# Optimization experiments

Hardware: AMD Instinct MI355X
Metric: run time of the kernel (lower is better)

The kernel has to match this reference:

```python
import jax, jax.numpy as jnp
import numpy as np

H, DK, DV, DM = 8, 64, 64, 512
MAX_REL = 32
REL_VOCAB = 2 * MAX_REL + 1  # use_neg_dist=True
TREE_VOCAB = 64


def rel_pos_matrix(length):
    r = jnp.arange(length)
    dist = r[None, :] - r[:, None]                      # [L, L]
    dist = jnp.clip(dist, -MAX_REL, MAX_REL)
    return dist + MAX_REL                               # use_neg_dist -> shift


def setup_inputs() -> dict:
    key = jax.random.key(0)
    ks = jax.random.split(key, 16)
    B, L = 8, 1024
    s = 0.02
    return {
        "key": jax.random.normal(ks[0], (B, L, DM), jnp.float32),
        "value": jax.random.normal(ks[1], (B, L, DM), jnp.float32),
        "query": jax.random.normal(ks[2], (B, L, DM), jnp.float32),
        "mask": jnp.zeros((B, L, L), jnp.bool_),
        "rel_matrix": jax.random.randint(ks[3], (B, L, L), 0, TREE_VOCAB, jnp.int32),
        "rel_mask": jax.random.uniform(ks[4], (B, L, L), jnp.float32),
        "Wk": jax.random.normal(ks[5], (DM, H * DK), jnp.float32) * s,
        "bk": jnp.zeros((H * DK,), jnp.float32),
        "Wq": jax.random.normal(ks[6], (DM, H * DK), jnp.float32) * s,
        "bq": jnp.zeros((H * DK,), jnp.float32),
        "Wv": jax.random.normal(ks[7], (DM, H * DV), jnp.float32) * s,
        "bv": jnp.zeros((H * DV,), jnp.float32),
        "Wo": jax.random.normal(ks[8], (H * DV, DM), jnp.float32) * s,
        "bo": jnp.zeros((DM,), jnp.float32),
        "rel_emb_k": jax.random.normal(ks[9], (REL_VOCAB, DK), jnp.float32) * s,
        "rel_emb_v": jax.random.normal(ks[10], (REL_VOCAB, DV), jnp.float32) * s,
        "tree_emb": jax.random.normal(ks[11], (TREE_VOCAB, H), jnp.float32) * s,
    }


def reference(key, value, query, mask, rel_matrix, rel_mask,
              Wk, bk, Wq, bq, Wv, bv, Wo, bo, rel_emb_k, rel_emb_v, tree_emb):
    B, L, _ = key.shape

    def shape(x, d):  # (B, L, H*d) -> (B, H, L, d)
        return x.reshape(B, L, H, d).transpose(0, 2, 1, 3)

    k = shape(key @ Wk + bk, DK)       # [B,H,L,DK]
    v = shape(value @ Wv + bv, DV)     # [B,H,L,DV]
    q = shape(query @ Wq + bq, DK)     # [B,H,L,DK]

    rp = rel_pos_matrix(L)             # [L,L] int constant
    rel_k = rel_emb_k[rp]              # [L,L,DK]
    rel_v = rel_emb_v[rp]              # [L,L,DV]

    q = q / jnp.sqrt(jnp.asarray(DK, q.dtype))
    scores = jnp.einsum("bhqd,bhkd->bhqk", q, k)
    # relative_matmul(q, rel_k, transpose=True)
    scores = scores + jnp.einsum("bhqd,qkd->bhqk", q, rel_k)
    # tree-relative bias: embedding lookup [B,Q,K,H] -> [B,H,Q,K], masked
    tree_bias = tree_emb[rel_matrix].transpose(0, 3, 1, 2)
    scores = scores + tree_bias * rel_mask[:, None, :, :]

    scores = scores.astype(jnp.float32)
    scores = jnp.where(mask[:, None, :, :], -1e18, scores)
    attn = jax.nn.softmax(scores, axis=-1).astype(q.dtype)  # [B,H,Q,K]

    ctx = jnp.einsum("bhqk,bhkd->bhqd", attn, v)
    # relative_matmul(attn, rel_v, transpose=False)
    ctx = ctx + jnp.einsum("bhqk,qkd->bhqd", attn, rel_v)

    ctx = ctx.transpose(0, 2, 1, 3).reshape(B, L, H * DV)
    return ctx @ Wo + bo
```

## Files before the change

### kernel.cpp

```cpp
#include <hip/hip_runtime.h>
#include <stdint.h>

using f32x4  = __attribute__((ext_vector_type(4))) float;
using short8 = __attribute__((ext_vector_type(8))) short;
typedef unsigned short u16;
typedef unsigned int   u32;


static __device__ __forceinline__ u16 f2bf(float f) {
  union { float f; u32 u; } v; v.f = f;
  u32 r = v.u + 0x7fffu + ((v.u >> 16) & 1u);
  return (u16)(r >> 16);
}
static __device__ __forceinline__ float bf2f(u16 u) {
  union { u32 u; float f; } v; v.u = ((u32)u) << 16;
  return v.f;
}
static __device__ __forceinline__ float fexp2(float x) {
  float r;
  asm("v_exp_f32 %0, %1" : "=v"(r) : "v"(x));
  return r;
}
static __device__ __forceinline__ u32 cvtpk(float a, float b) {
  u32 r;
  asm("v_cvt_pk_bf16_f32 %0, %1, %2" : "=v"(r) : "v"(a), "v"(b));
  return r;
}

#define GLDS16(g, l) __builtin_amdgcn_global_load_lds( \
    (const __attribute__((address_space(1))) u32*)(g), \
    (__attribute__((address_space(3))) u32*)(l), 16, 0, 0)

__global__ __launch_bounds__(256) void k_pre(
    const float* __restrict__ W0, const float* __restrict__ W1,
    const float* __restrict__ W2, const float* __restrict__ W3,
    u16* __restrict__ T0, u16* __restrict__ T1, u16* __restrict__ T2, u16* __restrict__ T3,
    const float* __restrict__ rk, const float* __restrict__ rv,
    u16* __restrict__ relk80, u16* __restrict__ relvT,
    const int* __restrict__ rm, const float* __restrict__ rw,
    const unsigned char* __restrict__ mk, u32* __restrict__ outp) {
  __shared__ float t[32][33];
  int bid = blockIdx.x, tid = threadIdx.x;
  if (bid < 1024) {
    int mat = bid >> 8, rem = bid & 255;
    const float* W = (mat == 0) ? W0 : (mat == 1) ? W1 : (mat == 2) ? W2 : W3;
    u16* T = (mat == 0) ? T0 : (mat == 1) ? T1 : (mat == 2) ? T2 : T3;
    int tx = tid & 31, ty = tid >> 5;
    int x0 = (rem & 15) * 32, y0 = (rem >> 4) * 32;
    #pragma unroll
    for (int i = 0; i < 4; i++)
      t[ty + i*8][tx] = W[(y0 + ty + i*8) * 512 + (x0 + tx)];
    __syncthreads();
    #pragma unroll
    for (int i = 0; i < 4; i++)
      T[(x0 + ty + i*8) * 512 + (y0 + tx)] = f2bf(t[tx][ty + i*8]);
  } else if (bid < 1068) {
    int i = (bid - 1024) * 256 + tid;
    if (i < 80*64) {
      int row = i >> 6;
      relk80[i] = (row < 65) ? f2bf(rk[i]) : (u16)0;
    }
    int j = i - 80*64;
    if (j >= 0 && j < 64*96) {
      int dv = j / 96, bk = j % 96;
      relvT[j] = (bk < 65) ? f2bf(rv[bk*64 + dv]) : (u16)0;
    }
  } else {
    int i = (bid - 1068) * 256 + tid;
    int4   r4 = ((const int4*)rm)[i];
    float4 w4 = ((const float4*)rw)[i];
    uchar4 m4 = ((const uchar4*)mk)[i];
    uint4 o;
    o.x = (u32)(r4.x & 63) | (m4.x ? 128u : 0u) | ((u32)f2bf(w4.x) << 16);
    o.y = (u32)(r4.y & 63) | (m4.y ? 128u : 0u) | ((u32)f2bf(w4.y) << 16);
    o.z = (u32)(r4.z & 63) | (m4.z ? 128u : 0u) | ((u32)f2bf(w4.z) << 16);
    o.w = (u32)(r4.w & 63) | (m4.w ? 128u : 0u) | ((u32)f2bf(w4.w) << 16);
    ((uint4*)outp)[i] = o;
  }
}

struct FArg { const float* A; const u16* Wt; const float* bias; void* out; int mode; float scale; };
struct GArg { const u16* A; const u16* Wt; const float* bias; void* out; int mode; float scale; };

__global__ __launch_bounds__(256, 3) void k_gemmf(FArg g0, FArg g1, FArg g2) {
  FArg ar = (blockIdx.z == 0) ? g0 : (blockIdx.z == 1) ? g1 : g2;
  __shared__ char smem_[34816];
  u16* As = (u16*)smem_;
  u16* Bs = (u16*)(smem_ + 16384);
  u16* Cs = (u16*)smem_;
  int tid = threadIdx.x, lane = tid & 63, wv = tid >> 6;
  int quad = lane >> 4, l15 = lane & 15;
  int n0 = blockIdx.x * 128, m0 = blockIdx.y * 128;
  int wm = (wv >> 1) * 64, wn = (wv & 1) * 64;
  f32x4 acc[4][4];
  #pragma unroll
  for (int i = 0; i < 4; i++)
    #pragma unroll
    for (int j = 0; j < 4; j++)
      acc[i][j] = (f32x4){0.f, 0.f, 0.f, 0.f};

  const float* Asrc = ar.A + (size_t)(m0 + (tid >> 1)) * 512 + (tid & 1) * 16;
  const u16* Bbase = ar.Wt + (size_t)n0 * 512;
  int c0 = wv * 128;

  float4 fA[4];
#define LOADA(kt) do { _Pragma("unroll") \
    for (int i = 0; i < 4; i++) fA[i] = *(const float4*)(Asrc + (kt)*32 + i*4); } while (0)
#define WRITEA(nb) do { \
    u32 w0 = cvtpk(fA[0].x, fA[0].y), w1 = cvtpk(fA[0].z, fA[0].w); \
    u32 w2 = cvtpk(fA[1].x, fA[1].y), w3 = cvtpk(fA[1].z, fA[1].w); \
    u32 w4 = cvtpk(fA[2].x, fA[2].y), w5 = cvtpk(fA[2].z, fA[2].w); \
    u32 w6 = cvtpk(fA[3].x, fA[3].y), w7 = cvtpk(fA[3].z, fA[3].w); \
    ((uint4*)&As[(nb)*4096 + tid*16])[0] = make_uint4(w0, w1, w2, w3); \
    ((uint4*)&As[(nb)*4096 + tid*16])[1] = make_uint4(w4, w5, w6, w7); } while (0)
#define GLDSB(kt, nb) do { _Pragma("unroll") \
    for (int i = 0; i < 2; i++) { \
      int c = c0 + i*64 + lane; \
      GLDS16(Bbase + (c >> 2)*512 + (kt)*32 + (c & 3)*8, &Bs[(nb)*4096 + (c0 + i*64)*8]); \
    } } while (0)

  LOADA(0);
  WRITEA(0);
  GLDSB(0, 0);

  for (int ks = 0; ks < 16; ks++) {
    int cur = ks & 1;
    if (ks < 15) LOADA(ks + 1);
    __syncthreads();
    if (ks < 15) { WRITEA(cur ^ 1); GLDSB(ks + 1, cur ^ 1); }
    int bs = cur * 4096;
    short8 af[4], bf[4];
    #pragma unroll
    for (int i = 0; i < 4; i++) af[i] = *(const short8*)&As[bs + (wm + i*16 + l15)*32 + quad*8];
    #pragma unroll
    for (int j = 0; j < 4; j++) bf[j] = *(const short8*)&Bs[bs + (wn + j*16 + l15)*32 + quad*8];
    __builtin_amdgcn_s_setprio(1);
    #pragma unroll
    for (int i = 0; i < 4; i++)
      #pragma unroll
      for (int j = 0; j < 4; j++)
        acc[i][j] = __builtin_amdgcn_mfma_f32_16x16x32_bf16(af[i], bf[j], acc[i][j], 0, 0, 0);
    __builtin_amdgcn_s_setprio(0);
  }
#undef LOADA
#undef WRITEA
#undef GLDSB
  __syncthreads();

  {
    #pragma unroll
    for (int i = 0; i < 4; i++)
      #pragma unroll
      for (int j = 0; j < 4; j++) {
        int nloc = wn + j*16 + l15;
        float bv = ar.bias[n0 + nloc];
        #pragma unroll
        for (int r = 0; r < 4; r++) {
          int mloc = wm + i*16 + quad*4 + r;
          float val = (acc[i][j][r] + bv) * ar.scale;
          if (ar.mode == 1) Cs[mloc*136 + nloc] = f2bf(val);
          else              Cs[nloc*136 + mloc] = f2bf(val);
        }
      }
    __syncthreads();
    int bb = m0 >> 10, hh0 = n0 >> 6, mbase = m0 & 1023;
    u16* outp = (u16*)ar.out;
    if (ar.mode == 1) {
      #pragma unroll
      for (int p = 0; p < 8; p++) {
        int mloc = (tid >> 4) + p*16, seg = tid & 15;
        int head = hh0 + (seg >> 3);
        size_t base = ((size_t)(bb*8 + head)*1024 + mbase)*64;
        *(short8*)(outp + base + (size_t)mloc*64 + (seg & 7)*8) =
            *(const short8*)&Cs[mloc*136 + seg*8];
      }
    } else {
      #pragma unroll
      for (int p = 0; p < 8; p++) {
        int nloc = (tid >> 4) + p*16, seg = tid & 15;
        int head = hh0 + (nloc >> 6), d = nloc & 63;
        size_t base = (size_t)(bb*8 + head)*64*1024 + mbase;
        *(short8*)(outp + base + (size_t)d*1024 + seg*8) =
            *(const short8*)&Cs[nloc*136 + seg*8];
      }
    }
  }
}

__global__ __launch_bounds__(256, 4) void k_gemm(GArg g0, GArg g1, GArg g2) {
  GArg ar = (blockIdx.z == 0) ? g0 : (blockIdx.z == 1) ? g1 : g2;
  __shared__ char smem_[34816];
  u16* As = (u16*)smem_;
  u16* Bs = (u16*)(smem_ + 16384);
  u16* Cs = (u16*)smem_;
  int tid = threadIdx.x, lane = tid & 63, wv = tid >> 6;
  int quad = lane >> 4, l15 = lane & 15;
  int n0 = blockIdx.x * 128, m0 = blockIdx.y * 128;
  int wm = (wv >> 1) * 64, wn = (wv & 1) * 64;
  f32x4 acc[4][4];
  #pragma unroll
  for (int i = 0; i < 4; i++)
    #pragma unroll
    for (int j = 0; j < 4; j++)
      acc[i][j] = (f32x4){0.f, 0.f, 0.f, 0.f};

  const u16* Abase = ar.A  + (size_t)m0 * 512;
  const u16* Bbase = ar.Wt + (size_t)n0 * 512;
  int c0 = wv * 128;

#define STAGEG(kt, nb) do { \
    _Pragma("unroll") \
    for (int i = 0; i < 2; i++) { \
      int c = c0 + i*64 + lane; \
      GLDS16(Abase + (c >> 2)*512 + (kt)*32 + (c & 3)*8, &As[(nb)*4096 + (c0 + i*64)*8]); \
      GLDS16(Bbase + (c >> 2)*512 + (kt)*32 + (c & 3)*8, &Bs[(nb)*4096 + (c0 + i*64)*8]); \
    } } while (0)

  STAGEG(0, 0);

  for (int ks = 0; ks < 16; ks++) {
    int cur = ks & 1;
    __syncthreads();
    if (ks < 15) STAGEG(ks + 1, cur ^ 1);
    int bs = cur * 4096;
    short8 af[4], bf[4];
    #pragma unroll
    for (int i = 0; i < 4; i++) af[i] = *(const short8*)&As[bs + (wm + i*16 + l15)*32 + quad*8];
    #pragma unroll
    for (int j = 0; j < 4; j++) bf[j] = *(const short8*)&Bs[bs + (wn + j*16 + l15)*32 + quad*8];
    __builtin_amdgcn_s_setprio(1);
    #pragma unroll
    for (int i = 0; i < 4; i++)
      #pragma unroll
      for (int j = 0; j < 4; j++)
        acc[i][j] = __builtin_amdgcn_mfma_f32_16x16x32_bf16(af[i], bf[j], acc[i][j], 0, 0, 0);
    __builtin_amdgcn_s_setprio(0);
  }
#undef STAGEG
  __syncthreads();

  if (ar.mode == 0) {
    #pragma unroll
    for (int i = 0; i < 4; i++)
      #pragma unroll
      for (int j = 0; j < 4; j++) {
        int ncol = n0 + wn + j*16 + l15;
        float bv = ar.bias[ncol];
        #pragma unroll
        for (int r = 0; r < 4; r++) {
          int m = m0 + wm + i*16 + quad*4 + r;
          ((float*)ar.out)[m*512 + ncol] = (acc[i][j][r] + bv) * ar.scale;
        }
      }
  } else {
    #pragma unroll
    for (int i = 0; i < 4; i++)
      #pragma unroll
      for (int j = 0; j < 4; j++) {
        int nloc = wn + j*16 + l15;
        float bv = ar.bias[n0 + nloc];
        #pragma unroll
        for (int r = 0; r < 4; r++) {
          int mloc = wm + i*16 + quad*4 + r;
          float val = (acc[i][j][r] + bv) * ar.scale;
          if (ar.mode == 1) Cs[mloc*136 + nloc] = f2bf(val);
          else              Cs[nloc*136 + mloc] = f2bf(val);
        }
      }
    __syncthreads();
    int bb = m0 >> 10, hh0 = n0 >> 6, mbase = m0 & 1023;
    u16* outp = (u16*)ar.out;
    if (ar.mode == 1) {
      #pragma unroll
      for (int p = 0; p < 8; p++) {
        int mloc = (tid >> 4) + p*16, seg = tid & 15;
        int head = hh0 + (seg >> 3);
        size_t base = ((size_t)(bb*8 + head)*1024 + mbase)*64;
        *(short8*)(outp + base + (size_t)mloc*64 + (seg & 7)*8) =
            *(const short8*)&Cs[mloc*136 + seg*8];
      }
    } else {
      #pragma unroll
      for (int p = 0; p < 8; p++) {
        int nloc = (tid >> 4) + p*16, seg = tid & 15;
        int head = hh0 + (nloc >> 6), d = nloc & 63;
        size_t base = (size_t)(bb*8 + head)*64*1024 + mbase;
        *(short8*)(outp + base + (size_t)d*1024 + seg*8) =
            *(const short8*)&Cs[nloc*136 + seg*8];
      }
    }
  }
}

__global__ __launch_bounds__(512, 4) void k_attn(
    const u16* __restrict__ qws, const u16* __restrict__ kws, const u16* __restrict__ vtws,
    const u16* __restrict__ relk80, const u16* __restrict__ relvT,
    const float* __restrict__ tree_emb, const u32* __restrict__ packed,
    u16* __restrict__ ctx) {
  __shared__ u16 Kb[2][2048];
  __shared__ u16 Vb[2][2048];
  __shared__ u16 qdotL[8*16*68];
  __shared__ u16 PB[8][16*96];
  __shared__ u16 Pl[8][16*40];

  int tid = threadIdx.x, lane = tid & 63, wv = tid >> 6;
  int quad = lane >> 4, l15 = lane & 15;
  int qb = blockIdx.x, h = blockIdx.y, b = blockIdx.z;
  int q0 = qb * 128 + wv * 16;

  float treev = tree_emb[lane * 8 + h] * 1.44269504f;

  #pragma unroll
  for (int i = 0; i < 12; i++) ((u32*)&PB[wv][0])[lane + i*64] = 0u;

  const u16* qp = qws  + (size_t)(b*8 + h)*(1024*64);
  const u16* kp = kws  + (size_t)(b*8 + h)*(1024*64);
  const u16* vp = vtws + (size_t)(b*8 + h)*(64*1024);
  const u32* pkb = packed + ((size_t)b << 20);

  int rk = (wv & 3)*8 + (lane >> 3);
  int swk = (((lane & 7)*8) ^ ((rk & 7) << 3));
  int rv = (wv & 3)*16 + (lane >> 2);
  const u16* vsrc = vp + (size_t)rv*1024 + (((lane & 3)*8) ^ ((rv & 3) << 3));

#define STAGE(kt, nb) do { \
    if (wv < 4) GLDS16(kp + (size_t)((kt)*32 + rk)*64 + swk, &Kb[nb][wv*512]); \
    else        GLDS16(vsrc + (kt)*32, &Vb[nb][(wv & 3)*512]); \
  } while (0)

  STAGE(0, 0);

  short8 aQ[2];
  #pragma unroll
  for (int kf = 0; kf < 2; kf++)
    aQ[kf] = *(const short8*)(qp + (q0 + l15)*64 + kf*32 + quad*8);

  float qd0[4], qd64[4];
  #pragma unroll
  for (int t = 0; t < 5; t++) {
    f32x4 C = (f32x4){0.f,0.f,0.f,0.f};
    #pragma unroll
    for (int kf = 0; kf < 2; kf++) {
      short8 bR = *(const short8*)(relk80 + (t*16 + l15)*64 + kf*32 + quad*8);
      C = __builtin_amdgcn_mfma_f32_16x16x32_bf16(aQ[kf], bR, C, 0, 0, 0);
    }
    if (t == 0) {
      #pragma unroll
      for (int r = 0; r < 4; r++) qd0[r] = __shfl(C[r], lane & 48, 64);
    }
    if (t == 4) {
      #pragma unroll
      for (int r = 0; r < 4; r++) qd64[r] = __shfl(C[r], lane & 48, 64);
    }
    int col = t*16 + l15;
    if (col < 65) {
      #pragma unroll
      for (int r = 0; r < 4; r++)
        qdotL[(wv*16 + quad*4 + r)*68 + col] = f2bf(C[r]);
    }
  }

  int t_lo = max(0, (q0 - 31) >> 5);
  int t_hi = min(31, (q0 + 46) >> 5);

  int sK = (l15 & 7) << 3;
  int kbo0 = l15*64 + ((quad*8) ^ sK);
  int kbo1 = l15*64 + (((4 + quad)*8) ^ sK);
  int vbo  = l15*32 + ((quad*8) ^ ((l15 & 3) << 3));

  u32 pk[8];
  #pragma unroll
  for (int e = 0; e < 8; e++)
    pk[e] = pkb[((q0 + quad*4 + (e & 3)) << 10) + (e >> 2)*16 + l15];

  f32x4 O[4];
  float rs[4], ts0[4], ts1[4];
  #pragma unroll
  for (int t = 0; t < 4; t++) O[t] = (f32x4){0.f,0.f,0.f,0.f};
  #pragma unroll
  for (int r = 0; r < 4; r++) { rs[r] = 0.f; ts0[r] = 0.f; ts1[r] = 0.f; }

  for (int jt = 0; jt < 32; ++jt) {
    int cur = jt & 1;
    int k0 = jt << 5;
    __syncthreads();
    if (jt < 31) STAGE(jt + 1, cur ^ 1);

    u32 pkc[8];
    #pragma unroll
    for (int e = 0; e < 8; e++) pkc[e] = pk[e];
    if (jt < 31) {
      int kn = (jt + 1) << 5;
      #pragma unroll
      for (int e = 0; e < 8; e++)
        pk[e] = pkb[((q0 + quad*4 + (e & 3)) << 10) + kn + (e >> 2)*16 + l15];
    }

    short8 kr00 = *(const short8*)&Kb[cur][kbo0];
    short8 kr01 = *(const short8*)&Kb[cur][kbo1];
    short8 kr10 = *(const short8*)&Kb[cur][1024 + kbo0];
    short8 kr11 = *(const short8*)&Kb[cur][1024 + kbo1];
    short8 vr[4];
    #pragma unroll
    for (int t = 0; t < 4; t++) vr[t] = *(const short8*)&Vb[cur][t*512 + vbo];

    f32x4 S0 = (f32x4){0.f,0.f,0.f,0.f}, S1 = (f32x4){0.f,0.f,0.f,0.f};
    __builtin_amdgcn_s_setprio(1);
    S0 = __builtin_amdgcn_mfma_f32_16x16x32_bf16(aQ[0], kr00, S0, 0, 0, 0);
    S0 = __builtin_amdgcn_mfma_f32_16x16x32_bf16(aQ[1], kr01, S0, 0, 0, 0);
    S1 = __builtin_amdgcn_mfma_f32_16x16x32_bf16(aQ[0], kr10, S1, 0, 0, 0);
    S1 = __builtin_amdgcn_mfma_f32_16x16x32_bf16(aQ[1], kr11, S1, 0, 0, 0);
    __builtin_amdgcn_s_setprio(0);
    f32x4 Scur[2] = { S0, S1 };

    if (jt < t_lo) {
      #pragma unroll
      for (int ct = 0; ct < 2; ct++) {
        float pv[4];
        #pragma unroll
        for (int r = 0; r < 4; r++) {
          u32 sg = pkc[ct*4 + r];
          float rw = __uint_as_float(sg & 0xffff0000u);
          float tb = __int_as_float(__builtin_amdgcn_ds_bpermute(
              (int)((sg & 63u) << 2), __float_as_int(treev)));
          float qm = (sg & 128u) ? -1e30f : qd0[r];
          float p = fexp2(__builtin_fmaf(tb, rw, Scur[ct][r] + qm));
          ts0[r] += p;
          pv[r] = p;
        }
        u32 c01 = cvtpk(pv[0], pv[1]), c23 = cvtpk(pv[2], pv[3]);
        u16* pl = &Pl[wv][(quad*4)*40 + ct*16 + l15];
        pl[0]   = (u16)c01; pl[40]  = (u16)(c01 >> 16);
        pl[80]  = (u16)c23; pl[120] = (u16)(c23 >> 16);
      }
    } else if (jt > t_hi) {
      #pragma unroll
      for (int ct = 0; ct < 2; ct++) {
        float pv[4];
        #pragma unroll
        for (int r = 0; r < 4; r++) {
          u32 sg = pkc[ct*4 + r];
          float rw = __uint_as_float(sg & 0xffff0000u);
          float tb = __int_as_float(__builtin_amdgcn_ds_bpermute(
              (int)((sg & 63u) << 2), __float_as_int(treev)));
          float qm = (sg & 128u) ? -1e30f : qd64[r];
          float p = fexp2(__builtin_fmaf(tb, rw, Scur[ct][r] + qm));
          ts1[r] += p;
          pv[r] = p;
        }
        u32 c01 = cvtpk(pv[0], pv[1]), c23 = cvtpk(pv[2], pv[3]);
        u16* pl = &Pl[wv][(quad*4)*40 + ct*16 + l15];
        pl[0]   = (u16)c01; pl[40]  = (u16)(c01 >> 16);
        pl[80]  = (u16)c23; pl[120] = (u16)(c23 >> 16);
      }
    } else {
      #pragma unroll
      for (int ct = 0; ct < 2; ct++) {
        float pv[4];
        #pragma unroll
        for (int r = 0; r < 4; r++) {
          int kloc = ct*16 + l15, qloc = quad*4 + r;
          int d = (k0 + kloc) - (q0 + qloc);
          int bucket = min(max(d + 32, 0), 64);
          u32 sg = pkc[ct*4 + r];
          float rw = __uint_as_float(sg & 0xffff0000u);
          float tb = __int_as_float(__builtin_amdgcn_ds_bpermute(
              (int)((sg & 63u) << 2), __float_as_int(treev)));
          float qd = bf2f(qdotL[(wv*16 + qloc)*68 + bucket]);
          float qm = (sg & 128u) ? -1e30f : qd;
          float p = fexp2(__builtin_fmaf(tb, rw, Scur[ct][r] + qm));
          if (d <= -32)      ts0[r] += p;
          else if (d >= 32)  ts1[r] += p;
          else             { rs[r] += p; PB[wv][qloc*96 + d + 32] = f2bf(p); }
          pv[r] = p;
        }
        u32 c01 = cvtpk(pv[0], pv[1]), c23 = cvtpk(pv[2], pv[3]);
        u16* pl = &Pl[wv][(quad*4)*40 + ct*16 + l15];
        pl[0]   = (u16)c01; pl[40]  = (u16)(c01 >> 16);
        pl[80]  = (u16)c23; pl[120] = (u16)(c23 >> 16);
      }
    }

    {
      short8 aP = *(const short8*)&Pl[wv][l15*40 + quad*8];
      __builtin_amdgcn_s_setprio(1);
      #pragma unroll
      for (int t = 0; t < 4; t++)
        O[t] = __builtin_amdgcn_mfma_f32_16x16x32_bf16(aP, vr[t], O[t], 0, 0, 0);
      __builtin_amdgcn_s_setprio(0);
    }
  }
#undef STAGE

  #pragma unroll
  for (int m = 1; m < 16; m <<= 1) {
    #pragma unroll
    for (int r = 0; r < 4; r++) {
      rs[r]  += __shfl_xor(rs[r],  m, 64);
      ts0[r] += __shfl_xor(ts0[r], m, 64);
      ts1[r] += __shfl_xor(ts1[r], m, 64);
    }
  }
  if (l15 == 0) {
    #pragma unroll
    for (int r = 0; r < 4; r++) {
      PB[wv][(quad*4 + r)*96 + 0]  = f2bf(ts0[r]);
      PB[wv][(quad*4 + r)*96 + 64] = f2bf(ts1[r]);
    }
  }

  {
    short8 aB[3];
    #pragma unroll
    for (int s = 0; s < 3; s++)
      aB[s] = *(const short8*)&PB[wv][l15*96 + s*32 + quad*8];
    #pragma unroll
    for (int t = 0; t < 4; t++)
      #pragma unroll
      for (int s = 0; s < 3; s++) {
        short8 bRV = *(const short8*)(relvT + (t*16 + l15)*96 + s*32 + quad*8);
        O[t] = __builtin_amdgcn_mfma_f32_16x16x32_bf16(aB[s], bRV, O[t], 0, 0, 0);
      }
  }

  {
    float inv[4];
    #pragma unroll
    for (int r = 0; r < 4; r++) inv[r] = 1.0f / (rs[r] + ts0[r] + ts1[r]);
    #pragma unroll
    for (int t = 0; t < 4; t++)
      #pragma unroll
      for (int r = 0; r < 4; r++) {
        int qg = q0 + quad*4 + r;
        ctx[(b*1024 + qg)*512 + h*64 + t*16 + l15] = f2bf(O[t][r] * inv[r]);
      }
  }
}

extern "C" void kernel_launch(void* const* d_in, const int* in_sizes, int n_in,
                              void* d_out, int out_size, void* d_ws, size_t ws_size,
                              hipStream_t stream) {
  const float* key   = (const float*)d_in[0];
  const float* value = (const float*)d_in[1];
  const float* query = (const float*)d_in[2];
  const unsigned char* maskp = (const unsigned char*)d_in[3];
  const int*   relm  = (const int*)d_in[4];
  const float* relw  = (const float*)d_in[5];
  const float* Wk = (const float*)d_in[6];
  const float* bk = (const float*)d_in[7];
  const float* Wq = (const float*)d_in[8];
  const float* bq = (const float*)d_in[9];
  const float* Wv = (const float*)d_in[10];
  const float* bv = (const float*)d_in[11];
  const float* Wo = (const float*)d_in[12];
  const float* bo = (const float*)d_in[13];
  const float* rek = (const float*)d_in[14];
  const float* rev = (const float*)d_in[15];
  const float* te  = (const float*)d_in[16];
  (void)in_sizes; (void)n_in; (void)out_size;

  char* w = (char*)d_ws;
  size_t off = 0;
  auto alloc = [&](size_t bytes) -> void* {
    void* p = w + off; off += (bytes + 255) & ~(size_t)255; return p;
  };
  u16* WkT = (u16*)alloc((size_t)512*512*2);
  u16* WqT = (u16*)alloc((size_t)512*512*2);
  u16* WvT = (u16*)alloc((size_t)512*512*2);
  u16* WoT = (u16*)alloc((size_t)512*512*2);
  u16* qws = (u16*)alloc((size_t)8*8*1024*64*2);
  u16* kws = (u16*)alloc((size_t)8*8*1024*64*2);
  u16* vt  = (u16*)alloc((size_t)8*8*1024*64*2);
  u32* packed = (u32*)alloc((size_t)8*1024*1024*4);
  u16* ctxb = (u16*)alloc((size_t)8192*512*2);
  u16* relk80 = (u16*)alloc((size_t)80*64*2);
  u16* relvT  = (u16*)alloc((size_t)64*96*2);
  if (off > ws_size) return;

  k_pre<<<9260, 256, 0, stream>>>(Wk, Wq, Wv, Wo, WkT, WqT, WvT, WoT,
                                  rek, rev, relk80, relvT,
                                  relm, relw, maskp, packed);

  FArg aq { query, WqT, bq, (void*)qws, 1, 0.18033688f };
  FArg ak { key,   WkT, bk, (void*)kws, 1, 1.0f };
  FArg av { value, WvT, bv, (void*)vt,  2, 1.0f };
  k_gemmf<<<dim3(4,64,3), 256, 0, stream>>>(aq, ak, av);

  k_attn<<<dim3(8,8,8), 512, 0, stream>>>(qws, kws, vt, relk80, relvT, te, packed, ctxb);

  GArg ao { ctxb, WoT, bo, d_out, 0, 1.0f };
  k_gemm<<<dim3(4,64,1), 256, 0, stream>>>(ao, ao, ao);
}
```

Baseline: 287.1 us.

## Move mask packing into QKV GEMM launch and deepen A-tile prefetch

The packing of rel_matrix, rel_mask and mask into one 32-bit word per element moves out of the preprocessing kernel and into extra blocks of the QKV projection GEMM launch. The bandwidth-bound packing can then run alongside the compute-bound GEMM blocks instead of before them. The GEMM main loop also gains a second fp32 A register buffer and is unrolled by two, so global loads for A are issued two k-steps ahead. This adds register pressure and places heavy and light blocks in a single grid.

```diff
diff --git a/kernel.cpp b/kernel.cpp
--- a/kernel.cpp
+++ b/kernel.cpp
@@ -36,9 +36,7 @@
     const float* __restrict__ W2, const float* __restrict__ W3,
     u16* __restrict__ T0, u16* __restrict__ T1, u16* __restrict__ T2, u16* __restrict__ T3,
     const float* __restrict__ rk, const float* __restrict__ rv,
-    u16* __restrict__ relk80, u16* __restrict__ relvT,
-    const int* __restrict__ rm, const float* __restrict__ rw,
-    const unsigned char* __restrict__ mk, u32* __restrict__ outp) {
+    u16* __restrict__ relk80, u16* __restrict__ relvT) {
   __shared__ float t[32][33];
   int bid = blockIdx.x, tid = threadIdx.x;
   if (bid < 1024) {
@@ -54,7 +52,7 @@
     #pragma unroll
     for (int i = 0; i < 4; i++)
       T[(x0 + ty + i*8) * 512 + (y0 + tx)] = f2bf(t[tx][ty + i*8]);
-  } else if (bid < 1068) {
+  } else {
     int i = (bid - 1024) * 256 + tid;
     if (i < 80*64) {
       int row = i >> 6;
@@ -65,8 +63,18 @@
       int dv = j / 96, bk = j % 96;
       relvT[j] = (bk < 65) ? f2bf(rv[bk*64 + dv]) : (u16)0;
     }
-  } else {
-    int i = (bid - 1068) * 256 + tid;
+  }
+}
+
+struct FArg { const float* A; const u16* Wt; const float* bias; void* out; int mode; float scale; };
+struct GArg { const u16* A; const u16* Wt; const float* bias; void* out; int mode; float scale; };
+
+__global__ __launch_bounds__(256, 3) void k_gemmf(FArg g0, FArg g1, FArg g2,
+    const int* __restrict__ rm, const float* __restrict__ rw,
+    const unsigned char* __restrict__ mk, u32* __restrict__ outp) {
+  int bid = blockIdx.x, tid = threadIdx.x;
+  if (bid >= 768) {
+    int i = (bid - 768) * 256 + tid;
     int4   r4 = ((const int4*)rm)[i];
     float4 w4 = ((const float4*)rw)[i];
     uchar4 m4 = ((const uchar4*)mk)[i];
@@ -76,21 +84,16 @@
     o.z = (u32)(r4.z & 63) | (m4.z ? 128u : 0u) | ((u32)f2bf(w4.z) << 16);
     o.w = (u32)(r4.w & 63) | (m4.w ? 128u : 0u) | ((u32)f2bf(w4.w) << 16);
     ((uint4*)outp)[i] = o;
-  }
-}
-
-struct FArg { const float* A; const u16* Wt; const float* bias; void* out; int mode; float scale; };
-struct GArg { const u16* A; const u16* Wt; const float* bias; void* out; int mode; float scale; };
-
-__global__ __launch_bounds__(256, 3) void k_gemmf(FArg g0, FArg g1, FArg g2) {
-  FArg ar = (blockIdx.z == 0) ? g0 : (blockIdx.z == 1) ? g1 : g2;
+    return;
+  }
+  FArg ar = (bid < 256) ? g0 : (bid < 512) ? g1 : g2;
   __shared__ char smem_[34816];
   u16* As = (u16*)smem_;
   u16* Bs = (u16*)(smem_ + 16384);
   u16* Cs = (u16*)smem_;
-  int tid = threadIdx.x, lane = tid & 63, wv = tid >> 6;
+  int lane = tid & 63, wv = tid >> 6;
   int quad = lane >> 4, l15 = lane & 15;
-  int n0 = blockIdx.x * 128, m0 = blockIdx.y * 128;
+  int n0 = (bid & 3) * 128, m0 = ((bid >> 2) & 63) * 128;
   int wm = (wv >> 1) * 64, wn = (wv & 1) * 64;
   f32x4 acc[4][4];
   #pragma unroll
@@ -103,14 +106,14 @@
   const u16* Bbase = ar.Wt + (size_t)n0 * 512;
   int c0 = wv * 128;
 
-  float4 fA[4];
-#define LOADA(kt) do { _Pragma("unroll") \
-    for (int i = 0; i < 4; i++) fA[i] = *(const float4*)(Asrc + (kt)*32 + i*4); } while (0)
-#define WRITEA(nb) do { \
-    u32 w0 = cvtpk(fA[0].x, fA[0].y), w1 = cvtpk(fA[0].z, fA[0].w); \
-    u32 w2 = cvtpk(fA[1].x, fA[1].y), w3 = cvtpk(fA[1].z, fA[1].w); \
-    u32 w4 = cvtpk(fA[2].x, fA[2].y), w5 = cvtpk(fA[2].z, fA[2].w); \
-    u32 w6 = cvtpk(fA[3].x, fA[3].y), w7 = cvtpk(fA[3].z, fA[3].w); \
+  float4 fA0[4], fA1[4];
+#define LOADA(fa, kt) do { _Pragma("unroll") \
+    for (int i = 0; i < 4; i++) fa[i] = *(const float4*)(Asrc + (kt)*32 + i*4); } while (0)
+#define WRITEA(fa, nb) do { \
+    u32 w0 = cvtpk(fa[0].x, fa[0].y), w1 = cvtpk(fa[0].z, fa[0].w); \
+    u32 w2 = cvtpk(fa[1].x, fa[1].y), w3 = cvtpk(fa[1].z, fa[1].w); \
+    u32 w4 = cvtpk(fa[2].x, fa[2].y), w5 = cvtpk(fa[2].z, fa[2].w); \
+    u32 w6 = cvtpk(fa[3].x, fa[3].y), w7 = cvtpk(fa[3].z, fa[3].w); \
     ((uint4*)&As[(nb)*4096 + tid*16])[0] = make_uint4(w0, w1, w2, w3); \
     ((uint4*)&As[(nb)*4096 + tid*16])[1] = make_uint4(w4, w5, w6, w7); } while (0)
 #define GLDSB(kt, nb) do { _Pragma("unroll") \
@@ -118,33 +121,42 @@
       int c = c0 + i*64 + lane; \
       GLDS16(Bbase + (c >> 2)*512 + (kt)*32 + (c & 3)*8, &Bs[(nb)*4096 + (c0 + i*64)*8]); \
     } } while (0)
-
-  LOADA(0);
-  WRITEA(0);
+#define MFMAS(nb) do { \
+    int bs = (nb) * 4096; \
+    short8 af[4], bf[4]; \
+    _Pragma("unroll") \
+    for (int i = 0; i < 4; i++) af[i] = *(const short8*)&As[bs + (wm + i*16 + l15)*32 + quad*8]; \
+    _Pragma("unroll") \
+    for (int j = 0; j < 4; j++) bf[j] = *(const short8*)&Bs[bs + (wn + j*16 + l15)*32 + quad*8]; \
+    __builtin_amdgcn_s_setprio(1); \
+    _Pragma("unroll") \
+    for (int i = 0; i < 4; i++) \
+      _Pragma("unroll") \
+      for (int j = 0; j < 4; j++) \
+        acc[i][j] = __builtin_amdgcn_mfma_f32_16x16x32_bf16(af[i], bf[j], acc[i][j], 0, 0, 0); \
+    __builtin_amdgcn_s_setprio(0); } while (0)
+
+  LOADA(fA0, 0);
+  WRITEA(fA0, 0);
   GLDSB(0, 0);
-
+  LOADA(fA1, 1);
+
+  #pragma unroll 2
   for (int ks = 0; ks < 16; ks++) {
-    int cur = ks & 1;
-    if (ks < 15) LOADA(ks + 1);
     __syncthreads();
-    if (ks < 15) { WRITEA(cur ^ 1); GLDSB(ks + 1, cur ^ 1); }
-    int bs = cur * 4096;
-    short8 af[4], bf[4];
-    #pragma unroll
-    for (int i = 0; i < 4; i++) af[i] = *(const short8*)&As[bs + (wm + i*16 + l15)*32 + quad*8];
-    #pragma unroll
-    for (int j = 0; j < 4; j++) bf[j] = *(const short8*)&Bs[bs + (wn + j*16 + l15)*32 + quad*8];
-    __builtin_amdgcn_s_setprio(1);
-    #pragma unroll
-    for (int i = 0; i < 4; i++)
-      #pragma unroll
-      for (int j = 0; j < 4; j++)
-        acc[i][j] = __builtin_amdgcn_mfma_f32_16x16x32_bf16(af[i], bf[j], acc[i][j], 0, 0, 0);
-    __builtin_amdgcn_s_setprio(0);
+    if (ks & 1) {
+      if (ks < 15) { WRITEA(fA0, (ks + 1) & 1); GLDSB(ks + 1, (ks + 1) & 1); }
+      if (ks < 14) LOADA(fA1, ks + 2);
+    } else {
+      if (ks < 15) { WRITEA(fA1, (ks + 1) & 1); GLDSB(ks + 1, (ks + 1) & 1); }
+      if (ks < 14) LOADA(fA0, ks + 2);
+    }
+    MFMAS(ks & 1);
   }
 #undef LOADA
 #undef WRITEA
 #undef GLDSB
+#undef MFMAS
   __syncthreads();
 
   {
@@ -164,14 +176,14 @@
       }
     __syncthreads();
     int bb = m0 >> 10, hh0 = n0 >> 6, mbase = m0 & 1023;
-    u16* outp = (u16*)ar.out;
+    u16* outp2 = (u16*)ar.out;
     if (ar.mode == 1) {
       #pragma unroll
       for (int p = 0; p < 8; p++) {
         int mloc = (tid >> 4) + p*16, seg = tid & 15;
         int head = hh0 + (seg >> 3);
         size_t base = ((size_t)(bb*8 + head)*1024 + mbase)*64;
-        *(short8*)(outp + base + (size_t)mloc*64 + (seg & 7)*8) =
+        *(short8*)(outp2 + base + (size_t)mloc*64 + (seg & 7)*8) =
             *(const short8*)&Cs[mloc*136 + seg*8];
       }
     } else {
@@ -180,7 +192,7 @@
         int nloc = (tid >> 4) + p*16, seg = tid & 15;
         int head = hh0 + (nloc >> 6), d = nloc & 63;
         size_t base = (size_t)(bb*8 + head)*64*1024 + mbase;
-        *(short8*)(outp + base + (size_t)d*1024 + seg*8) =
+        *(short8*)(outp2 + base + (size_t)d*1024 + seg*8) =
             *(const short8*)&Cs[nloc*136 + seg*8];
       }
     }
@@ -577,14 +589,13 @@
   u16* relvT  = (u16*)alloc((size_t)64*96*2);
   if (off > ws_size) return;
 
-  k_pre<<<9260, 256, 0, stream>>>(Wk, Wq, Wv, Wo, WkT, WqT, WvT, WoT,
-                                  rek, rev, relk80, relvT,
-                                  relm, relw, maskp, packed);
+  k_pre<<<1068, 256, 0, stream>>>(Wk, Wq, Wv, Wo, WkT, WqT, WvT, WoT,
+                                  rek, rev, relk80, relvT);
 
   FArg aq { query, WqT, bq, (void*)qws, 1, 0.18033688f };
   FArg ak { key,   WkT, bk, (void*)kws, 1, 1.0f };
   FArg av { value, WvT, bv, (void*)vt,  2, 1.0f };
-  k_gemmf<<<dim3(4,64,3), 256, 0, stream>>>(aq, ak, av);
+  k_gemmf<<<8960, 256, 0, stream>>>(aq, ak, av, relm, relw, maskp, packed);
 
   k_attn<<<dim3(8,8,8), 512, 0, stream>>>(qws, kws, vt, relk80, relvT, te, packed, ctxb);
 
```

Measured after the change: 284.5 us. Within noise of the previous version (-0.9%).
